# Kernel optimization log

Measured on AMD Instinct MI355X. Metric: run time of the kernel, lower is better.

## Reference

```python
import jax, jax.numpy as jnp
import numpy as np

D_MODEL = 2048
D_STATE = 128
D_CONV = 4
EXPAND = 2
HEADDIM = 64
NGROUPS = 1
CHUNK = 256
D_INNER = EXPAND * D_MODEL               # 4096 (= d_ssm, since d_ssm=None)
NHEADS = D_INNER // HEADDIM              # 64
CONV_DIM = D_INNER + 2 * NGROUPS * D_STATE   # 4352
D_IN_PROJ = 2 * D_INNER + 2 * NGROUPS * D_STATE + NHEADS  # 8512
EPS = 1e-5


def setup_inputs() -> dict:
    key = jax.random.key(0)
    ks = jax.random.split(key, 8)
    B, L = 2, 4096
    u = jax.random.normal(ks[0], (B, L, D_MODEL), jnp.float32)
    in_proj_kernel = jax.random.normal(ks[1], (D_MODEL, D_IN_PROJ), jnp.float32) * (1.0 / np.sqrt(D_MODEL))
    conv1d_weight = jax.random.normal(ks[2], (CONV_DIM, D_CONV), jnp.float32) * (1.0 / np.sqrt(D_CONV))
    conv1d_bias = jnp.zeros((CONV_DIM,), jnp.float32)
    # dt_bias: inverse-softplus of log-uniform dt in [dt_min, dt_max]
    uu = jax.random.uniform(ks[3], (NHEADS,), jnp.float32)
    dt = jnp.exp(uu * (np.log(0.1) - np.log(0.001)) + np.log(0.001))
    dt = jnp.maximum(dt, 1e-4)
    dt_bias = dt + jnp.log(-jnp.expm1(-dt))
    # A_log: log of uniform(1, 16)
    A_log = jnp.log(jax.random.uniform(ks[4], (NHEADS,), jnp.float32, minval=1.0, maxval=16.0))
    D = jnp.ones((NHEADS,), jnp.float32)
    norm_weight = jnp.ones((D_INNER,), jnp.float32)
    out_proj_kernel = jax.random.normal(ks[5], (D_INNER, D_MODEL), jnp.float32) * (1.0 / np.sqrt(D_INNER))
    return {"u": u, "in_proj_kernel": in_proj_kernel, "conv1d_weight": conv1d_weight,
            "conv1d_bias": conv1d_bias, "dt_bias": dt_bias, "A_log": A_log, "D": D,
            "norm_weight": norm_weight, "out_proj_kernel": out_proj_kernel}


def _segsum(x):
    """x: (..., L). Returns (..., L, L) with seg[i,j] = sum_{k=j+1..i} x_k for i>=j, -inf above diag."""
    T = x.shape[-1]
    cs = jnp.cumsum(x, axis=-1)
    seg = cs[..., :, None] - cs[..., None, :]
    mask = jnp.tril(jnp.ones((T, T), dtype=bool))
    return jnp.where(mask, seg, -jnp.inf)


def _causal_conv1d_silu(x, w, b):
    """Depthwise causal conv. x: (B, C, L), w: (C, K), b: (C,)."""
    K = w.shape[-1]
    Lx = x.shape[-1]
    xp = jnp.pad(x, ((0, 0), (0, 0), (K - 1, 0)))
    y = b[None, :, None]
    for k in range(K):  # K=4, tiny static loop
        y = y + w[None, :, k:k + 1] * xp[:, :, k:k + Lx]
    return jax.nn.silu(y)


def _mamba2_forward(u, in_proj_kernel, conv1d_weight, conv1d_bias, dt_bias, A_log, D,
                    norm_weight, out_proj_kernel):
    B_, L, _ = u.shape
    zxbcdt = u @ in_proj_kernel  # (B, L, d_in_proj); d_mlp = 0 so no z0/x0
    z = zxbcdt[..., :D_INNER]
    xBC = zxbcdt[..., D_INNER:D_INNER + CONV_DIM]
    dt = zxbcdt[..., D_INNER + CONV_DIM:]  # (B, L, H)

    xBC = _causal_conv1d_silu(jnp.transpose(xBC, (0, 2, 1)), conv1d_weight, conv1d_bias)
    xBC = jnp.transpose(xBC, (0, 2, 1))

    x = xBC[..., :D_INNER].reshape(B_, L, NHEADS, HEADDIM)
    Bm = xBC[..., D_INNER:D_INNER + NGROUPS * D_STATE].reshape(B_, L, NGROUPS, D_STATE)
    Cm = xBC[..., D_INNER + NGROUPS * D_STATE:].reshape(B_, L, NGROUPS, D_STATE)

    dt = jax.nn.softplus(dt + dt_bias)         # (B, L, H); dt_limit=(0,inf) => no clamp
    A = -jnp.exp(A_log)                        # (H,)

    nc = L // CHUNK
    r = NHEADS // NGROUPS
    # chunked views
    xc = x.reshape(B_, nc, CHUNK, NGROUPS, r, HEADDIM)
    dtc = dt.reshape(B_, nc, CHUNK, NGROUPS, r)
    Bc = Bm.reshape(B_, nc, CHUNK, NGROUPS, D_STATE)
    Cc = Cm.reshape(B_, nc, CHUNK, NGROUPS, D_STATE)
    xdt = xc * dtc[..., None]                  # dt-discretized input

    dA = dtc * A.reshape(NGROUPS, r)           # (B, nc, CL, g, r)
    dA = jnp.transpose(dA, (0, 3, 4, 1, 2))    # (B, g, r, nc, CL)
    A_cs = jnp.cumsum(dA, axis=-1)

    # intra-chunk (diagonal blocks)
    Lmat = jnp.exp(_segsum(dA))                # (B, g, r, nc, CL, CL)
    Y_diag = jnp.einsum('bclgn,bcsgn,bgrcls,bcsgrp->bclgrp', Cc, Bc, Lmat, xdt)

    # per-chunk end states
    decay_states = jnp.exp(A_cs[..., -1:] - A_cs)  # (B, g, r, nc, CL)
    states = jnp.einsum('bcsgn,bgrcs,bcsgrp->bcgrpn', Bc, decay_states, xdt)

    # inter-chunk recurrence over nc chunks
    chunk_decay = jnp.exp(A_cs[..., -1])       # (B, g, r, nc)
    states_t = jnp.moveaxis(states, 1, 0)      # (nc, B, g, r, p, n)
    decay_t = jnp.moveaxis(chunk_decay, -1, 0) # (nc, B, g, r)

    def step(S, inp):
        d, st = inp
        S_new = S * d[..., None, None] + st
        return S_new, S  # emit state at start of each chunk

    S0 = jnp.zeros(states_t.shape[1:], states_t.dtype)
    _, prev_states = jax.lax.scan(step, S0, (decay_t, states_t))
    prev_states = jnp.moveaxis(prev_states, 0, 1)  # (B, nc, g, r, p, n)

    state_decay = jnp.exp(A_cs)                # (B, g, r, nc, CL)
    Y_off = jnp.einsum('bclgn,bcgrpn,bgrcl->bclgrp', Cc, prev_states, state_decay)

    Y = (Y_diag + Y_off).reshape(B_, nc, CHUNK, NHEADS, HEADDIM)
    Y = Y + x.reshape(B_, nc, CHUNK, NHEADS, HEADDIM) * D[:, None]  # D skip (D_has_hdim=False)
    y = Y.reshape(B_, L, D_INNER)

    # RMSNormGated (norm_before_gate=False): norm(y * silu(z)) * weight
    y = y * jax.nn.silu(z)
    y = y * jax.lax.rsqrt(jnp.mean(y * y, axis=-1, keepdims=True) + EPS) * norm_weight

    return y @ out_proj_kernel


def reference(u, in_proj_kernel, conv1d_weight, conv1d_bias, dt_bias, A_log, D,
              norm_weight, out_proj_kernel):
    return _mamba2_forward(u, in_proj_kernel, conv1d_weight, conv1d_bias, dt_bias, A_log, D,
                           norm_weight, out_proj_kernel)
```

## Files before the change

### kernel.cpp

```cpp
#include <hip/hip_runtime.h>
#include <cstddef>
#include <cstdint>
#include <math.h>

#define BATCH   2
#define LSEQ    4096
#define DMODEL  2048
#define DSTATE  128
#define HDIM    64
#define CHUNK   256
#define DINNER  4096
#define NHEADS  64
#define CONVD   4352
#define DPROJ   8512
#define NCHUNK  16
#define MROWS   (BATCH*LSEQ)
#define NPAD2   8704

typedef unsigned short bf16_t;
union U4 { uint4 u; unsigned short s[8]; };

typedef __attribute__((ext_vector_type(8))) short short8;
typedef __attribute__((ext_vector_type(4))) float f32x4;
union S8 { short8 v; unsigned short s[8]; };

__device__ __forceinline__ float b2f(unsigned short u) {
    union { unsigned int i; float f; } v; v.i = ((unsigned int)u) << 16; return v.f;
}
__device__ __forceinline__ unsigned short f2b(float f) {
    union { float f; unsigned int i; } v; v.f = f;
    unsigned int r = v.i + 0x7fffu + ((v.i >> 16) & 1u);
    return (unsigned short)(r >> 16);
}

__device__ __forceinline__ void gload_lds16(const void* g, void* l) {
    auto gp = reinterpret_cast<const __attribute__((address_space(1))) unsigned int*>(
        reinterpret_cast<uintptr_t>(g));
    auto lp = reinterpret_cast<__attribute__((address_space(3))) unsigned int*>(
        reinterpret_cast<uintptr_t>(l));
    __builtin_amdgcn_global_load_lds(gp, lp, 16, 0, 0);
}

__global__ __launch_bounds__(256) void cast_bf16(const float* __restrict__ in,
                                                 bf16_t* __restrict__ out, size_t n8) {
    size_t i = (size_t)blockIdx.x * 256 + threadIdx.x;
    if (i >= n8) return;
    const float4 a = *(const float4*)(in + i * 8);
    const float4 b = *(const float4*)(in + i * 8 + 4);
    U4 o;
    o.s[0]=f2b(a.x); o.s[1]=f2b(a.y); o.s[2]=f2b(a.z); o.s[3]=f2b(a.w);
    o.s[4]=f2b(b.x); o.s[5]=f2b(b.y); o.s[6]=f2b(b.z); o.s[7]=f2b(b.w);
    *(uint4*)(out + i * 8) = o.u;
}

__global__ __launch_bounds__(256) void transpose_cast(const float* __restrict__ W,
                                                      bf16_t* __restrict__ Bt,
                                                      int K, int N) {
    __shared__ float t[32][33];
    const int bx = blockIdx.x;
    const int by = blockIdx.y;
    const int tx = threadIdx.x, ty = threadIdx.y;
    const int n = bx * 32 + tx;
#pragma unroll
    for (int r = 0; r < 4; ++r) {
        int k = by * 32 + ty + r * 8;
        t[ty + r * 8][tx] = (n < N) ? W[(size_t)k * N + n] : 0.f;
    }
    __syncthreads();
#pragma unroll
    for (int r = 0; r < 4; ++r) {
        int nn = bx * 32 + ty + r * 8;
        Bt[(size_t)nn * K + by * 32 + tx] = f2b(t[tx][ty + r * 8]);
    }
}

#define MM(a,b,c) __builtin_amdgcn_mfma_f32_16x16x32_bf16(a,b,c,0,0,0)

template<bool BF16OUT>
__global__ __launch_bounds__(512, 2) void gemm256(const bf16_t* __restrict__ A,
                                                  const bf16_t* __restrict__ Bt,
                                                  void* __restrict__ Cout,
                                                  int GX, int N, int K,
                                                  int lda, int ldb, int ldc) {
    __shared__ __align__(16) bf16_t Asm[2][256 * 64];
    __shared__ __align__(16) bf16_t Bsm[2][256 * 64];
    const int tid  = threadIdx.x;
    const int wid  = tid >> 6;
    const int lane = tid & 63;
    const int wm = wid >> 2;
    const int wn = wid & 3;

    const int nwg = gridDim.x;
    const int wg  = blockIdx.x;
    const int q8 = nwg >> 3, r8 = nwg & 7;
    const int xcd = wg & 7, lo = wg >> 3;
    const int swz = (xcd < r8 ? xcd * (q8 + 1) : r8 * (q8 + 1) + (xcd - r8) * q8) + lo;
    const int bm = (swz / GX) * 256;
    const int bn = (swz % GX) * 256;

    const int fr  = lane & 15;
    const int kx0 = ((((lane >> 4))     ^ (lane & 7)) * 8);
    const int kx1 = ((((lane >> 4) + 4) ^ (lane & 7)) * 8);
    const int laneA  = lane >> 3;
    const int chunkS = ((lane & 7) ^ (lane >> 3)) * 8;

    f32x4 acc[8][4];
#pragma unroll
    for (int i = 0; i < 8; ++i)
#pragma unroll
        for (int j = 0; j < 4; ++j) acc[i][j] = (f32x4){0.f, 0.f, 0.f, 0.f};

    short8 b00, b01, b10, b11, b20, b21, b30, b31;

#define STAGE_A(d, t, h) do { \
    const int r0_ = (h) * 128 + wid * 16; \
    gload_lds16(A + (size_t)(bm + r0_ +     laneA) * lda + (t) * 64 + chunkS, &Asm[d][(r0_    ) * 64]); \
    gload_lds16(A + (size_t)(bm + r0_ + 8 + laneA) * lda + (t) * 64 + chunkS, &Asm[d][(r0_ + 8) * 64]); \
} while (0)
#define STAGE_B(d, t, h) do { \
    const int r0_ = (h) * 128 + wid * 16; \
    gload_lds16(Bt + (size_t)(bn + r0_ +     laneA) * ldb + (t) * 64 + chunkS, &Bsm[d][(r0_    ) * 64]); \
    gload_lds16(Bt + (size_t)(bn + r0_ + 8 + laneA) * ldb + (t) * 64 + chunkS, &Bsm[d][(r0_ + 8) * 64]); \
} while (0)

#define PHASE(curb, qq, DOVM, ...) do { \
    const bf16_t* Ab_ = &Asm[curb][(wm * 128 + (qq) * 32 + fr) * 64]; \
    short8 a00 = *(const short8*)(Ab_ + kx0); \
    short8 a01 = *(const short8*)(Ab_ + kx1); \
    short8 a10 = *(const short8*)(Ab_ + 16 * 64 + kx0); \
    short8 a11 = *(const short8*)(Ab_ + 16 * 64 + kx1); \
    if ((qq) == 0) { \
        const bf16_t* Bb_ = &Bsm[curb][(wn * 64 + fr) * 64]; \
        b00 = *(const short8*)(Bb_ + kx0);           b01 = *(const short8*)(Bb_ + kx1); \
        b10 = *(const short8*)(Bb_ + 16 * 64 + kx0); b11 = *(const short8*)(Bb_ + 16 * 64 + kx1); \
        b20 = *(const short8*)(Bb_ + 32 * 64 + kx0); b21 = *(const short8*)(Bb_ + 32 * 64 + kx1); \
        b30 = *(const short8*)(Bb_ + 48 * 64 + kx0); b31 = *(const short8*)(Bb_ + 48 * 64 + kx1); \
    } \
    __VA_ARGS__ \
    __builtin_amdgcn_sched_barrier(0); \
    __builtin_amdgcn_s_barrier(); \
    asm volatile("s_waitcnt lgkmcnt(0)" ::: "memory"); \
    __builtin_amdgcn_sched_barrier(0); \
    __builtin_amdgcn_s_setprio(1); \
    acc[(qq)*2  ][0] = MM(a00, b00, acc[(qq)*2  ][0]); acc[(qq)*2  ][0] = MM(a01, b01, acc[(qq)*2  ][0]); \
    acc[(qq)*2  ][1] = MM(a00, b10, acc[(qq)*2  ][1]); acc[(qq)*2  ][1] = MM(a01, b11, acc[(qq)*2  ][1]); \
    acc[(qq)*2  ][2] = MM(a00, b20, acc[(qq)*2  ][2]); acc[(qq)*2  ][2] = MM(a01, b21, acc[(qq)*2  ][2]); \
    acc[(qq)*2  ][3] = MM(a00, b30, acc[(qq)*2  ][3]); acc[(qq)*2  ][3] = MM(a01, b31, acc[(qq)*2  ][3]); \
    acc[(qq)*2+1][0] = MM(a10, b00, acc[(qq)*2+1][0]); acc[(qq)*2+1][0] = MM(a11, b01, acc[(qq)*2+1][0]); \
    acc[(qq)*2+1][1] = MM(a10, b10, acc[(qq)*2+1][1]); acc[(qq)*2+1][1] = MM(a11, b11, acc[(qq)*2+1][1]); \
    acc[(qq)*2+1][2] = MM(a10, b20, acc[(qq)*2+1][2]); acc[(qq)*2+1][2] = MM(a11, b21, acc[(qq)*2+1][2]); \
    acc[(qq)*2+1][3] = MM(a10, b30, acc[(qq)*2+1][3]); acc[(qq)*2+1][3] = MM(a11, b31, acc[(qq)*2+1][3]); \
    __builtin_amdgcn_s_setprio(0); \
    __builtin_amdgcn_sched_barrier(0); \
    if ((DOVM) == 1)      asm volatile("s_waitcnt vmcnt(4)" ::: "memory"); \
    else if ((DOVM) == 2) asm volatile("s_waitcnt vmcnt(0)" ::: "memory"); \
    __builtin_amdgcn_s_barrier(); \
} while (0)

    const int NT = K >> 6;
    const int NI = NT >> 1;

    STAGE_A(0, 0, 0); STAGE_A(0, 0, 1);
    STAGE_B(0, 0, 0); STAGE_B(0, 0, 1);
    STAGE_B(1, 1, 0); STAGE_B(1, 1, 1);
    asm volatile("s_waitcnt vmcnt(4)" ::: "memory");
    __builtin_amdgcn_s_barrier();

    for (int i = 0; i < NI - 1; ++i) {
        const int t0 = 2 * i;
        PHASE(0, 0, 0, STAGE_A(1, t0 + 1, 0); );
        PHASE(0, 1, 0, STAGE_A(1, t0 + 1, 1); );
        PHASE(0, 2, 0, STAGE_B(0, t0 + 2, 0); );
        PHASE(0, 3, 1, STAGE_B(0, t0 + 2, 1); );
        PHASE(1, 0, 0, STAGE_A(0, t0 + 2, 0); );
        PHASE(1, 1, 0, STAGE_A(0, t0 + 2, 1); );
        PHASE(1, 2, 0, STAGE_B(1, t0 + 3, 0); );
        PHASE(1, 3, 1, STAGE_B(1, t0 + 3, 1); );
    }
    PHASE(0, 0, 0, STAGE_A(1, NT - 1, 0); );
    PHASE(0, 1, 0, STAGE_A(1, NT - 1, 1); );
    PHASE(0, 2, 0, );
    PHASE(0, 3, 2, );
    PHASE(1, 0, 0, );
    PHASE(1, 1, 0, );
    PHASE(1, 2, 0, );
    PHASE(1, 3, 0, );

#undef PHASE
#undef STAGE_A
#undef STAGE_B

    const int crow4 = (lane >> 4) * 4, ccol = lane & 15;
#pragma unroll
    for (int mr = 0; mr < 8; ++mr)
#pragma unroll
        for (int nf = 0; nf < 4; ++nf) {
            const int gr = bm + wm * 128 + mr * 16 + crow4;
            const int gc = bn + wn * 64 + nf * 16 + ccol;
            if (gc < N) {
                if (BF16OUT) {
                    bf16_t* C = (bf16_t*)Cout;
#pragma unroll
                    for (int r = 0; r < 4; ++r)
                        C[(size_t)(gr + r) * ldc + gc] = f2b(acc[mr][nf][r]);
                } else {
                    float* C = (float*)Cout;
#pragma unroll
                    for (int r = 0; r < 4; ++r)
                        C[(size_t)(gr + r) * ldc + gc] = acc[mr][nf][r];
                }
            }
        }
}

__global__ __launch_bounds__(256) void conv_silu(const bf16_t* __restrict__ zx,
                                                 const float* __restrict__ w,
                                                 const float* __restrict__ bias,
                                                 bf16_t* __restrict__ xconv) {
    const int c0 = (blockIdx.x * 256 + threadIdx.x) * 8;
    if (c0 >= CONVD) return;
    const int row0 = blockIdx.y * 4;
    float4 wv[8];
#pragma unroll
    for (int j = 0; j < 8; ++j) wv[j] = *(const float4*)(w + (size_t)(c0 + j) * 4);
    float bs[8];
    {
        float4 q0 = *(const float4*)(bias + c0), q1 = *(const float4*)(bias + c0 + 4);
        bs[0]=q0.x; bs[1]=q0.y; bs[2]=q0.z; bs[3]=q0.w;
        bs[4]=q1.x; bs[5]=q1.y; bs[6]=q1.z; bs[7]=q1.w;
    }
    U4 zin[7];
#pragma unroll
    for (int d = 0; d < 7; ++d) {
        int rr = row0 - 3 + d;
        if (rr >= 0) zin[d].u = *(const uint4*)(zx + (size_t)rr * DPROJ + DINNER + c0);
        else         zin[d].u = make_uint4(0, 0, 0, 0);
    }
    const int l0 = row0 & (LSEQ - 1);
#pragma unroll
    for (int r = 0; r < 4; ++r) {
        U4 o;
#pragma unroll
        for (int j = 0; j < 8; ++j) {
            float a = bs[j];
            const float* wj = (const float*)&wv[j];
#pragma unroll
            for (int k = 0; k < 4; ++k)
                if (l0 + r + k - 3 >= 0)
                    a += wj[k] * b2f(zin[r + k].s[j]);
            o.s[j] = f2b(a / (1.f + __expf(-a)));
        }
        *(uint4*)(xconv + (size_t)(row0 + r) * CONVD + c0) = o.u;
    }
}

__global__ void dt_softplus(const bf16_t* __restrict__ zx, const float* __restrict__ dt_bias,
                            float* __restrict__ dts) {
    const int idx = blockIdx.x * 256 + threadIdx.x;
    const int h = idx & 63;
    const int row = idx >> 6;
    float x = b2f(zx[(size_t)row * DPROJ + DINNER + CONVD + h]) + dt_bias[h];
    dts[idx] = (x > 20.f) ? x : log1pf(__expf(x));
}

__global__ __launch_bounds__(256) void chunk_state(const bf16_t* __restrict__ xconv,
                                                   const float* __restrict__ dts,
                                                   const float* __restrict__ A_log,
                                                   float* __restrict__ A_cs_g,
                                                   float* __restrict__ states) {
    const int h = blockIdx.x, cc = blockIdx.y, b = blockIdx.z;
    const int tid = threadIdx.x, wid = tid >> 6, lane = tid & 63;
    __shared__ float cs[CHUNK];
    __shared__ __align__(16) bf16_t xwT[HDIM][CHUNK + 8];
    __shared__ __align__(16) bf16_t BvT[DSTATE][CHUNK + 8];
    const int rowbase = b * LSEQ + cc * CHUNK;

    const float dtv = dts[(size_t)(rowbase + tid) * NHEADS + h];
    const float Ah = -__expf(A_log[h]);
    cs[tid] = dtv * Ah;
    __syncthreads();
    for (int off = 1; off < CHUNK; off <<= 1) {
        float v = (tid >= off) ? cs[tid - off] : 0.f;
        __syncthreads();
        cs[tid] += v;
        __syncthreads();
    }
    const size_t acs_base = ((size_t)((b * NCHUNK + cc) * NHEADS + h)) * CHUNK;
    A_cs_g[acs_base + tid] = cs[tid];
    const float w_ = __expf(cs[CHUNK - 1] - cs[tid]) * dtv;

    {
        const bf16_t* xr = xconv + (size_t)(rowbase + tid) * CONVD + h * HDIM;
#pragma unroll
        for (int p8 = 0; p8 < 8; ++p8) {
            U4 v; v.u = *(const uint4*)(xr + p8 * 8);
#pragma unroll
            for (int j = 0; j < 8; ++j) xwT[p8 * 8 + j][tid] = f2b(b2f(v.s[j]) * w_);
        }
        const bf16_t* br = xconv + (size_t)(rowbase + tid) * CONVD + DINNER;
#pragma unroll
        for (int n8 = 0; n8 < 16; ++n8) {
            U4 v; v.u = *(const uint4*)(br + n8 * 8);
#pragma unroll
            for (int j = 0; j < 8; ++j) BvT[n8 * 8 + j][tid] = v.s[j];
        }
    }
    __syncthreads();

    const int fr = lane & 15, fk8 = (lane >> 4) * 8;
    f32x4 acc[4][2];
#pragma unroll
    for (int i = 0; i < 4; ++i)
#pragma unroll
        for (int j = 0; j < 2; ++j) acc[i][j] = (f32x4){0.f, 0.f, 0.f, 0.f};

#pragma unroll
    for (int ks = 0; ks < 8; ++ks) {
        const int k0 = ks * 32 + fk8;
        short8 av[4], bv[2];
#pragma unroll
        for (int mi = 0; mi < 4; ++mi)
            av[mi] = *(const short8*)&xwT[mi * 16 + fr][k0];
#pragma unroll
        for (int ni = 0; ni < 2; ++ni)
            bv[ni] = *(const short8*)&BvT[wid * 32 + ni * 16 + fr][k0];
#pragma unroll
        for (int mi = 0; mi < 4; ++mi)
#pragma unroll
            for (int ni = 0; ni < 2; ++ni)
                acc[mi][ni] = __builtin_amdgcn_mfma_f32_16x16x32_bf16(
                    av[mi], bv[ni], acc[mi][ni], 0, 0, 0);
    }
    float* st = states + ((size_t)((b * NCHUNK + cc) * NHEADS + h)) * (HDIM * DSTATE);
    const int crow4 = (lane >> 4) * 4, ccol = lane & 15;
#pragma unroll
    for (int mi = 0; mi < 4; ++mi)
#pragma unroll
        for (int ni = 0; ni < 2; ++ni)
#pragma unroll
            for (int r = 0; r < 4; ++r)
                st[(size_t)(mi * 16 + crow4 + r) * DSTATE + wid * 32 + ni * 16 + ccol] =
                    acc[mi][ni][r];
}

__global__ __launch_bounds__(256) void state_scan(float* __restrict__ states,
                                                  const float* __restrict__ A_cs_g) {
    const int h = blockIdx.x, piece = blockIdx.y, b = blockIdx.z;
    const int tid = threadIdx.x;
    float S[4] = {0.f, 0.f, 0.f, 0.f};
    for (int c = 0; c < NCHUNK; ++c) {
        const size_t sbase = ((size_t)((b * NCHUNK + c) * NHEADS + h)) * (HDIM * DSTATE)
                           + (size_t)piece * 1024;
        const float decay = __expf(A_cs_g[((size_t)((b * NCHUNK + c) * NHEADS + h)) * CHUNK + CHUNK - 1]);
#pragma unroll
        for (int i = 0; i < 4; ++i) {
            size_t idx = sbase + i * 256 + tid;
            float v = states[idx];
            states[idx] = S[i];
            S[i] = S[i] * decay + v;
        }
    }
}

__global__ __launch_bounds__(256) void cb_mfma(const bf16_t* __restrict__ xconv,
                                               float* __restrict__ CBg) {
    const int pi = blockIdx.x, cc = blockIdx.y, b = blockIdx.z;
    const int lt = (pi >= 6) ? 3 : (pi >= 3) ? 2 : (pi >= 1) ? 1 : 0;
    const int st = pi - ((lt * (lt + 1)) >> 1);
    const int tid = threadIdx.x, wid = tid >> 6, lane = tid & 63;
    const int rowbase = b * LSEQ + cc * CHUNK;
    const int fr = lane & 15, fk8 = (lane >> 4) * 8;

    const bf16_t* Crow = xconv + (size_t)(rowbase + lt * 64 + wid * 16) * CONVD + DINNER + DSTATE;
    const bf16_t* Brow = xconv + (size_t)(rowbase + st * 64) * CONVD + DINNER;

    f32x4 acc[4];
#pragma unroll
    for (int i = 0; i < 4; ++i) acc[i] = (f32x4){0.f, 0.f, 0.f, 0.f};

#pragma unroll
    for (int kk = 0; kk < 4; ++kk) {
        const int k0 = kk * 32 + fk8;
        short8 av = *(const short8*)(Crow + (size_t)fr * CONVD + k0);
        short8 bv[4];
#pragma unroll
        for (int ni = 0; ni < 4; ++ni)
            bv[ni] = *(const short8*)(Brow + (size_t)(ni * 16 + fr) * CONVD + k0);
#pragma unroll
        for (int ni = 0; ni < 4; ++ni)
            acc[ni] = __builtin_amdgcn_mfma_f32_16x16x32_bf16(av, bv[ni], acc[ni], 0, 0, 0);
    }
    float* out = CBg + ((size_t)(b * NCHUNK + cc)) * CHUNK * CHUNK;
    const int crow4 = (lane >> 4) * 4, ccol = lane & 15;
#pragma unroll
    for (int ni = 0; ni < 4; ++ni)
#pragma unroll
        for (int r = 0; r < 4; ++r)
            out[(size_t)(lt * 64 + wid * 16 + crow4 + r) * CHUNK + st * 64 + ni * 16 + ccol] =
                acc[ni][r];
}

__global__ __launch_bounds__(256) void y_mfma(const bf16_t* __restrict__ xconv,
                                              const float* __restrict__ dts,
                                              const float* __restrict__ A_cs_g,
                                              const float* __restrict__ prev_states,
                                              const float* __restrict__ CBg,
                                              const float* __restrict__ Dv,
                                              bf16_t* __restrict__ zx) {
    const int h = blockIdx.x, cc = blockIdx.y, b = blockIdx.z;
    const int tid = threadIdx.x, wid = tid >> 6, lane = tid & 63;
    __shared__ float Acs_s[CHUNK];
    __shared__ __align__(16) bf16_t xdtT[HDIM][CHUNK + 8];
    __shared__ __align__(16) bf16_t Pt[4][64][72];
    const int rowbase = b * LSEQ + cc * CHUNK;
    const size_t acs_base = ((size_t)((b * NCHUNK + cc) * NHEADS + h)) * CHUNK;

    Acs_s[tid] = A_cs_g[acs_base + tid];
    {
        float dtv = dts[(size_t)(rowbase + tid) * NHEADS + h];
        const bf16_t* xr = xconv + (size_t)(rowbase + tid) * CONVD + h * HDIM;
#pragma unroll
        for (int p8 = 0; p8 < 8; ++p8) {
            U4 v; v.u = *(const uint4*)(xr + p8 * 8);
#pragma unroll
            for (int j = 0; j < 8; ++j)
                xdtT[p8 * 8 + j][tid] = f2b(b2f(v.s[j]) * dtv);
        }
    }
    __syncthreads();

    const int fr = lane & 15, fk8 = (lane >> 4) * 8;
    f32x4 acc[4][4];
#pragma unroll
    for (int i = 0; i < 4; ++i)
#pragma unroll
        for (int j = 0; j < 4; ++j) acc[i][j] = (f32x4){0.f, 0.f, 0.f, 0.f};

    const bf16_t* Crow = xconv + (size_t)(rowbase + wid * 64) * CONVD + DINNER + DSTATE;
    const float* prev = prev_states + ((size_t)((b * NCHUNK + cc) * NHEADS + h)) * (HDIM * DSTATE);
#pragma unroll
    for (int kk = 0; kk < 4; ++kk) {
        const int k0 = kk * 32 + fk8;
        short8 av[4], bv[4];
#pragma unroll
        for (int mi = 0; mi < 4; ++mi)
            av[mi] = *(const short8*)(Crow + (size_t)(mi * 16 + fr) * CONVD + k0);
#pragma unroll
        for (int ni = 0; ni < 4; ++ni) {
            const float* pr = prev + (size_t)(ni * 16 + fr) * DSTATE + k0;
            float4 f0 = *(const float4*)pr;
            float4 f1 = *(const float4*)(pr + 4);
            S8 t;
            t.s[0]=f2b(f0.x); t.s[1]=f2b(f0.y); t.s[2]=f2b(f0.z); t.s[3]=f2b(f0.w);
            t.s[4]=f2b(f1.x); t.s[5]=f2b(f1.y); t.s[6]=f2b(f1.z); t.s[7]=f2b(f1.w);
            bv[ni] = t.v;
        }
#pragma unroll
        for (int mi = 0; mi < 4; ++mi)
#pragma unroll
            for (int ni = 0; ni < 4; ++ni)
                acc[mi][ni] = __builtin_amdgcn_mfma_f32_16x16x32_bf16(
                    av[mi], bv[ni], acc[mi][ni], 0, 0, 0);
    }

    const int crow4 = (lane >> 4) * 4, ccol = lane & 15;
#pragma unroll
    for (int mi = 0; mi < 4; ++mi) {
        float e[4];
#pragma unroll
        for (int r = 0; r < 4; ++r)
            e[r] = __expf(Acs_s[wid * 64 + mi * 16 + crow4 + r]);
#pragma unroll
        for (int ni = 0; ni < 4; ++ni)
#pragma unroll
            for (int r = 0; r < 4; ++r) acc[mi][ni][r] *= e[r];
    }

    const float* cbb = CBg + ((size_t)(b * NCHUNK + cc)) * CHUNK * CHUNK;
    for (int st = 0; st <= wid; ++st) {
        const int s0 = st * 64;
        const float as_l = Acs_s[s0 + lane];
        __asm__ volatile("s_waitcnt lgkmcnt(0)" ::: "memory");
        __builtin_amdgcn_sched_barrier(0);
        for (int e = 0; e < 64; ++e) {
            const int gl = wid * 64 + e;
            float cbv = cbb[(size_t)gl * CHUNK + s0 + lane];
            float pv = cbv * __expf(Acs_s[gl] - as_l);
            if (st == wid && (s0 + lane) > gl) pv = 0.f;
            Pt[wid][e][lane] = f2b(pv);
        }
        __asm__ volatile("s_waitcnt lgkmcnt(0)" ::: "memory");
        __builtin_amdgcn_sched_barrier(0);
#pragma unroll
        for (int ks = 0; ks < 2; ++ks) {
            short8 av[4], bv[4];
#pragma unroll
            for (int mi = 0; mi < 4; ++mi)
                av[mi] = *(const short8*)&Pt[wid][mi * 16 + fr][ks * 32 + fk8];
#pragma unroll
            for (int ni = 0; ni < 4; ++ni)
                bv[ni] = *(const short8*)&xdtT[ni * 16 + fr][s0 + ks * 32 + fk8];
#pragma unroll
            for (int mi = 0; mi < 4; ++mi)
#pragma unroll
                for (int ni = 0; ni < 4; ++ni)
                    acc[mi][ni] = __builtin_amdgcn_mfma_f32_16x16x32_bf16(
                        av[mi], bv[ni], acc[mi][ni], 0, 0, 0);
        }
    }

    const float Dh = Dv[h];
#pragma unroll
    for (int mi = 0; mi < 4; ++mi)
#pragma unroll
        for (int ni = 0; ni < 4; ++ni) {
            const int p = ni * 16 + ccol;
#pragma unroll
            for (int r = 0; r < 4; ++r) {
                const int l = wid * 64 + mi * 16 + crow4 + r;
                const size_t row = (size_t)rowbase + l;
                float xr = b2f(xconv[row * CONVD + h * HDIM + p]);
                float zv = b2f(zx[row * DPROJ + h * HDIM + p]);
                float y = (acc[mi][ni][r] + xr * Dh) * (zv / (1.f + __expf(-zv)));
                zx[row * DPROJ + DINNER + h * HDIM + p] = f2b(y);
            }
        }
}

__global__ __launch_bounds__(256) void rmsnorm(bf16_t* __restrict__ zx, const float* __restrict__ nw) {
    const int row = blockIdx.x;
    const int tid = threadIdx.x;
    float fv[16];
    float ss = 0.f;
#pragma unroll
    for (int it = 0; it < 2; ++it) {
        int j0 = (it * 256 + tid) * 8;
        U4 v; v.u = *(const uint4*)(zx + (size_t)row * DPROJ + DINNER + j0);
#pragma unroll
        for (int j = 0; j < 8; ++j) { float f = b2f(v.s[j]); fv[it * 8 + j] = f; ss += f * f; }
    }
#pragma unroll
    for (int off = 32; off > 0; off >>= 1) ss += __shfl_down(ss, off, 64);
    __shared__ float red[4];
    if ((tid & 63) == 0) red[tid >> 6] = ss;
    __syncthreads();
    float tot = red[0] + red[1] + red[2] + red[3];
    float inv = rsqrtf(tot / (float)DINNER + 1e-5f);
#pragma unroll
    for (int it = 0; it < 2; ++it) {
        int j0 = (it * 256 + tid) * 8;
        U4 o;
#pragma unroll
        for (int j = 0; j < 8; ++j) o.s[j] = f2b(fv[it * 8 + j] * inv * nw[j0 + j]);
        *(uint4*)(zx + (size_t)row * DPROJ + j0) = o.u;
    }
}

extern "C" void kernel_launch(void* const* d_in, const int* in_sizes, int n_in,
                              void* d_out, int out_size, void* d_ws, size_t ws_size,
                              hipStream_t stream) {
    const float* u       = (const float*)d_in[0];
    const float* Win     = (const float*)d_in[1];
    const float* convw   = (const float*)d_in[2];
    const float* convb   = (const float*)d_in[3];
    const float* dt_bias = (const float*)d_in[4];
    const float* A_log   = (const float*)d_in[5];
    const float* Dv      = (const float*)d_in[6];
    const float* nw      = (const float*)d_in[7];
    const float* Wout    = (const float*)d_in[8];
    float* out = (float*)d_out;

    bf16_t* zx    = (bf16_t*)d_ws;
    bf16_t* xconv = zx + (size_t)MROWS * DPROJ;
    float*  dts   = (float*)(xconv + (size_t)MROWS * CONVD);
    float*  acs   = dts + (size_t)MROWS * NHEADS;
    float*  cb    = acs + (size_t)BATCH * NCHUNK * NHEADS * CHUNK;

    bf16_t* Abf    = xconv;
    bf16_t* Btin   = (bf16_t*)d_out;
    float*  states = (float*)d_out;
    bf16_t* Btout  = xconv;

    cast_bf16<<<(MROWS * DMODEL / 8 + 255) / 256, 256, 0, stream>>>(u, Abf, (size_t)MROWS * DMODEL / 8);
    transpose_cast<<<dim3(NPAD2 / 32, DMODEL / 32), dim3(32, 8), 0, stream>>>(Win, Btin, DMODEL, DPROJ);
    gemm256<true><<<dim3((NPAD2 / 256) * (MROWS / 256)), 512, 0, stream>>>(
        Abf, Btin, zx, NPAD2 / 256, DPROJ, DMODEL, DMODEL, DMODEL, DPROJ);
    conv_silu<<<dim3((CONVD / 8 + 255) / 256, MROWS / 4), 256, 0, stream>>>(zx, convw, convb, xconv);
    dt_softplus<<<dim3(MROWS * NHEADS / 256), 256, 0, stream>>>(zx, dt_bias, dts);
    chunk_state<<<dim3(NHEADS, NCHUNK, BATCH), 256, 0, stream>>>(xconv, dts, A_log, acs, states);
    state_scan<<<dim3(NHEADS, 8, BATCH), 256, 0, stream>>>(states, acs);
    cb_mfma<<<dim3(10, NCHUNK, BATCH), 256, 0, stream>>>(xconv, cb);
    y_mfma<<<dim3(NHEADS, NCHUNK, BATCH), 256, 0, stream>>>(xconv, dts, acs, states, cb, Dv, zx);
    transpose_cast<<<dim3(DMODEL / 32, DINNER / 32), dim3(32, 8), 0, stream>>>(Wout, Btout, DINNER, DMODEL);
    rmsnorm<<<MROWS, 256, 0, stream>>>(zx, nw);
    gemm256<false><<<dim3((DMODEL / 256) * (MROWS / 256)), 512, 0, stream>>>(
        zx, Btout, out, DMODEL / 256, DMODEL, DINNER, DPROJ, DINNER, DMODEL);
}
```

Before: 776.3 us.

## Triple-buffer A tiles in GEMM and reorder MFMAs to avoid accumulator stalls

The bf16 GEMM now keeps three LDS buffers for A instead of two, so A loads are issued two k-steps ahead and more global loads stay in flight (vmcnt relaxed from 4 to 8). The MFMA sequence is reordered so the two k-halves hitting the same accumulator are no longer back-to-back, hiding MFMA dependency latency. The explicit lgkmcnt(0) wait before the MFMAs is dropped, leaving LDS-read waits to the compiler. LDS use rises to 160 KB per block, which fills the CU's LDS and risks tighter scheduling or occupancy limits.

```diff
diff --git a/kernel.cpp b/kernel.cpp
--- a/kernel.cpp
+++ b/kernel.cpp
@@ -82,8 +82,9 @@
                                                   void* __restrict__ Cout,
                                                   int GX, int N, int K,
                                                   int lda, int ldb, int ldc) {
-    __shared__ __align__(16) bf16_t Asm[2][256 * 64];
-    __shared__ __align__(16) bf16_t Bsm[2][256 * 64];
+    __shared__ __align__(16) bf16_t Asm[3 * 256 * 64];
+    __shared__ __align__(16) bf16_t Bsm[2 * 256 * 64];
+    const int TSZ = 256 * 64;
     const int tid  = threadIdx.x;
     const int wid  = tid >> 6;
     const int lane = tid & 63;
@@ -112,25 +113,25 @@
 
     short8 b00, b01, b10, b11, b20, b21, b30, b31;
 
-#define STAGE_A(d, t, h) do { \
+#define STAGE_A(dst, t, h) do { \
     const int r0_ = (h) * 128 + wid * 16; \
-    gload_lds16(A + (size_t)(bm + r0_ +     laneA) * lda + (t) * 64 + chunkS, &Asm[d][(r0_    ) * 64]); \
-    gload_lds16(A + (size_t)(bm + r0_ + 8 + laneA) * lda + (t) * 64 + chunkS, &Asm[d][(r0_ + 8) * 64]); \
+    gload_lds16(A + (size_t)(bm + r0_ +     laneA) * lda + (t) * 64 + chunkS, (dst) + (r0_    ) * 64); \
+    gload_lds16(A + (size_t)(bm + r0_ + 8 + laneA) * lda + (t) * 64 + chunkS, (dst) + (r0_ + 8) * 64); \
 } while (0)
-#define STAGE_B(d, t, h) do { \
+#define STAGE_B(dst, t, h) do { \
     const int r0_ = (h) * 128 + wid * 16; \
-    gload_lds16(Bt + (size_t)(bn + r0_ +     laneA) * ldb + (t) * 64 + chunkS, &Bsm[d][(r0_    ) * 64]); \
-    gload_lds16(Bt + (size_t)(bn + r0_ + 8 + laneA) * ldb + (t) * 64 + chunkS, &Bsm[d][(r0_ + 8) * 64]); \
+    gload_lds16(Bt + (size_t)(bn + r0_ +     laneA) * ldb + (t) * 64 + chunkS, (dst) + (r0_    ) * 64); \
+    gload_lds16(Bt + (size_t)(bn + r0_ + 8 + laneA) * ldb + (t) * 64 + chunkS, (dst) + (r0_ + 8) * 64); \
 } while (0)
 
-#define PHASE(curb, qq, DOVM, ...) do { \
-    const bf16_t* Ab_ = &Asm[curb][(wm * 128 + (qq) * 32 + fr) * 64]; \
+#define PHASE(APTR, BPTR, qq, DOVM, ...) do { \
+    const bf16_t* Ab_ = (APTR) + (wm * 128 + (qq) * 32 + fr) * 64; \
     short8 a00 = *(const short8*)(Ab_ + kx0); \
     short8 a01 = *(const short8*)(Ab_ + kx1); \
     short8 a10 = *(const short8*)(Ab_ + 16 * 64 + kx0); \
     short8 a11 = *(const short8*)(Ab_ + 16 * 64 + kx1); \
     if ((qq) == 0) { \
-        const bf16_t* Bb_ = &Bsm[curb][(wn * 64 + fr) * 64]; \
+        const bf16_t* Bb_ = (BPTR) + (wn * 64 + fr) * 64; \
         b00 = *(const short8*)(Bb_ + kx0);           b01 = *(const short8*)(Bb_ + kx1); \
         b10 = *(const short8*)(Bb_ + 16 * 64 + kx0); b11 = *(const short8*)(Bb_ + 16 * 64 + kx1); \
         b20 = *(const short8*)(Bb_ + 32 * 64 + kx0); b21 = *(const short8*)(Bb_ + 32 * 64 + kx1); \
@@ -139,20 +140,26 @@
     __VA_ARGS__ \
     __builtin_amdgcn_sched_barrier(0); \
     __builtin_amdgcn_s_barrier(); \
-    asm volatile("s_waitcnt lgkmcnt(0)" ::: "memory"); \
-    __builtin_amdgcn_sched_barrier(0); \
     __builtin_amdgcn_s_setprio(1); \
-    acc[(qq)*2  ][0] = MM(a00, b00, acc[(qq)*2  ][0]); acc[(qq)*2  ][0] = MM(a01, b01, acc[(qq)*2  ][0]); \
-    acc[(qq)*2  ][1] = MM(a00, b10, acc[(qq)*2  ][1]); acc[(qq)*2  ][1] = MM(a01, b11, acc[(qq)*2  ][1]); \
-    acc[(qq)*2  ][2] = MM(a00, b20, acc[(qq)*2  ][2]); acc[(qq)*2  ][2] = MM(a01, b21, acc[(qq)*2  ][2]); \
-    acc[(qq)*2  ][3] = MM(a00, b30, acc[(qq)*2  ][3]); acc[(qq)*2  ][3] = MM(a01, b31, acc[(qq)*2  ][3]); \
-    acc[(qq)*2+1][0] = MM(a10, b00, acc[(qq)*2+1][0]); acc[(qq)*2+1][0] = MM(a11, b01, acc[(qq)*2+1][0]); \
-    acc[(qq)*2+1][1] = MM(a10, b10, acc[(qq)*2+1][1]); acc[(qq)*2+1][1] = MM(a11, b11, acc[(qq)*2+1][1]); \
-    acc[(qq)*2+1][2] = MM(a10, b20, acc[(qq)*2+1][2]); acc[(qq)*2+1][2] = MM(a11, b21, acc[(qq)*2+1][2]); \
-    acc[(qq)*2+1][3] = MM(a10, b30, acc[(qq)*2+1][3]); acc[(qq)*2+1][3] = MM(a11, b31, acc[(qq)*2+1][3]); \
+    acc[(qq)*2  ][0] = MM(a00, b00, acc[(qq)*2  ][0]); \
+    acc[(qq)*2  ][1] = MM(a00, b10, acc[(qq)*2  ][1]); \
+    acc[(qq)*2  ][2] = MM(a00, b20, acc[(qq)*2  ][2]); \
+    acc[(qq)*2  ][3] = MM(a00, b30, acc[(qq)*2  ][3]); \
+    acc[(qq)*2+1][0] = MM(a10, b00, acc[(qq)*2+1][0]); \
+    acc[(qq)*2+1][1] = MM(a10, b10, acc[(qq)*2+1][1]); \
+    acc[(qq)*2+1][2] = MM(a10, b20, acc[(qq)*2+1][2]); \
+    acc[(qq)*2+1][3] = MM(a10, b30, acc[(qq)*2+1][3]); \
+    acc[(qq)*2  ][0] = MM(a01, b01, acc[(qq)*2  ][0]); \
+    acc[(qq)*2  ][1] = MM(a01, b11, acc[(qq)*2  ][1]); \
+    acc[(qq)*2  ][2] = MM(a01, b21, acc[(qq)*2  ][2]); \
+    acc[(qq)*2  ][3] = MM(a01, b31, acc[(qq)*2  ][3]); \
+    acc[(qq)*2+1][0] = MM(a11, b01, acc[(qq)*2+1][0]); \
+    acc[(qq)*2+1][1] = MM(a11, b11, acc[(qq)*2+1][1]); \
+    acc[(qq)*2+1][2] = MM(a11, b21, acc[(qq)*2+1][2]); \
+    acc[(qq)*2+1][3] = MM(a11, b31, acc[(qq)*2+1][3]); \
     __builtin_amdgcn_s_setprio(0); \
     __builtin_amdgcn_sched_barrier(0); \
-    if ((DOVM) == 1)      asm volatile("s_waitcnt vmcnt(4)" ::: "memory"); \
+    if ((DOVM) == 1)      asm volatile("s_waitcnt vmcnt(8)" ::: "memory"); \
     else if ((DOVM) == 2) asm volatile("s_waitcnt vmcnt(0)" ::: "memory"); \
     __builtin_amdgcn_s_barrier(); \
 } while (0)
@@ -160,31 +167,41 @@
     const int NT = K >> 6;
     const int NI = NT >> 1;
 
-    STAGE_A(0, 0, 0); STAGE_A(0, 0, 1);
-    STAGE_B(0, 0, 0); STAGE_B(0, 0, 1);
-    STAGE_B(1, 1, 0); STAGE_B(1, 1, 1);
-    asm volatile("s_waitcnt vmcnt(4)" ::: "memory");
+    STAGE_A(Asm, 0, 0);       STAGE_A(Asm, 0, 1);
+    STAGE_B(Bsm, 0, 0);       STAGE_B(Bsm, 0, 1);
+    STAGE_A(Asm + TSZ, 1, 0); STAGE_A(Asm + TSZ, 1, 1);
+    STAGE_B(Bsm + TSZ, 1, 0); STAGE_B(Bsm + TSZ, 1, 1);
+    asm volatile("s_waitcnt vmcnt(8)" ::: "memory");
     __builtin_amdgcn_s_barrier();
 
+    int ac = 0;
     for (int i = 0; i < NI - 1; ++i) {
         const int t0 = 2 * i;
-        PHASE(0, 0, 0, STAGE_A(1, t0 + 1, 0); );
-        PHASE(0, 1, 0, STAGE_A(1, t0 + 1, 1); );
-        PHASE(0, 2, 0, STAGE_B(0, t0 + 2, 0); );
-        PHASE(0, 3, 1, STAGE_B(0, t0 + 2, 1); );
-        PHASE(1, 0, 0, STAGE_A(0, t0 + 2, 0); );
-        PHASE(1, 1, 0, STAGE_A(0, t0 + 2, 1); );
-        PHASE(1, 2, 0, STAGE_B(1, t0 + 3, 0); );
-        PHASE(1, 3, 1, STAGE_B(1, t0 + 3, 1); );
-    }
-    PHASE(0, 0, 0, STAGE_A(1, NT - 1, 0); );
-    PHASE(0, 1, 0, STAGE_A(1, NT - 1, 1); );
-    PHASE(0, 2, 0, );
-    PHASE(0, 3, 2, );
-    PHASE(1, 0, 0, );
-    PHASE(1, 1, 0, );
-    PHASE(1, 2, 0, );
-    PHASE(1, 3, 0, );
+        bf16_t* At  = Asm + ac * TSZ;
+        bf16_t* At1 = Asm + ((ac + 1) % 3) * TSZ;
+        bf16_t* At2 = Asm + ((ac + 2) % 3) * TSZ;
+        PHASE(At, Bsm, 0, 0, STAGE_A(At2, t0 + 2, 0); );
+        PHASE(At, Bsm, 1, 0, STAGE_A(At2, t0 + 2, 1); );
+        PHASE(At, Bsm, 2, 0, STAGE_B(Bsm, t0 + 2, 0); );
+        PHASE(At, Bsm, 3, 1, STAGE_B(Bsm, t0 + 2, 1); );
+        PHASE(At1, Bsm + TSZ, 0, 0, STAGE_A(At, t0 + 3, 0); );
+        PHASE(At1, Bsm + TSZ, 1, 0, STAGE_A(At, t0 + 3, 1); );
+        PHASE(At1, Bsm + TSZ, 2, 0, STAGE_B(Bsm + TSZ, t0 + 3, 0); );
+        PHASE(At1, Bsm + TSZ, 3, 1, STAGE_B(Bsm + TSZ, t0 + 3, 1); );
+        ac = (ac + 2) % 3;
+    }
+    {
+        bf16_t* At  = Asm + ac * TSZ;
+        bf16_t* At1 = Asm + ((ac + 1) % 3) * TSZ;
+        PHASE(At, Bsm, 0, 0, );
+        PHASE(At, Bsm, 1, 0, );
+        PHASE(At, Bsm, 2, 0, );
+        PHASE(At, Bsm, 3, 2, );
+        PHASE(At1, Bsm + TSZ, 0, 0, );
+        PHASE(At1, Bsm + TSZ, 1, 0, );
+        PHASE(At1, Bsm + TSZ, 2, 0, );
+        PHASE(At1, Bsm + TSZ, 3, 0, );
+    }
 
 #undef PHASE
 #undef STAGE_A
```

After: 782.4 us. About the same (+0.8%).

## Interleave chunk rows across waves in y_mfma to balance causal work

Applied to the files above, without the earlier changes.

Reassigns the 256 chunk rows in y_mfma so each wave takes a 16-row slice of every 64-row block instead of one contiguous 64-row block. The triangular intra-chunk work is then spread evenly across the four waves rather than leaving the last wave with four times the work of the first. The P staging buffer shrinks to 16 rows per wave. Separately, an explicit LDS wait after the barrier in the GEMM phase macro is removed, relying on compiler-inserted waits, which trims stalls but relaxes an explicit ordering guarantee.

```diff
diff --git a/kernel.cpp b/kernel.cpp
--- a/kernel.cpp
+++ b/kernel.cpp
@@ -139,8 +139,6 @@
     __VA_ARGS__ \
     __builtin_amdgcn_sched_barrier(0); \
     __builtin_amdgcn_s_barrier(); \
-    asm volatile("s_waitcnt lgkmcnt(0)" ::: "memory"); \
-    __builtin_amdgcn_sched_barrier(0); \
     __builtin_amdgcn_s_setprio(1); \
     acc[(qq)*2  ][0] = MM(a00, b00, acc[(qq)*2  ][0]); acc[(qq)*2  ][0] = MM(a01, b01, acc[(qq)*2  ][0]); \
     acc[(qq)*2  ][1] = MM(a00, b10, acc[(qq)*2  ][1]); acc[(qq)*2  ][1] = MM(a01, b11, acc[(qq)*2  ][1]); \
@@ -411,7 +409,7 @@
     const int tid = threadIdx.x, wid = tid >> 6, lane = tid & 63;
     __shared__ float Acs_s[CHUNK];
     __shared__ __align__(16) bf16_t xdtT[HDIM][CHUNK + 8];
-    __shared__ __align__(16) bf16_t Pt[4][64][72];
+    __shared__ __align__(16) bf16_t Pt[4][16][72];
     const int rowbase = b * LSEQ + cc * CHUNK;
     const size_t acs_base = ((size_t)((b * NCHUNK + cc) * NHEADS + h)) * CHUNK;
 
@@ -436,7 +434,7 @@
 #pragma unroll
         for (int j = 0; j < 4; ++j) acc[i][j] = (f32x4){0.f, 0.f, 0.f, 0.f};
 
-    const bf16_t* Crow = xconv + (size_t)(rowbase + wid * 64) * CONVD + DINNER + DSTATE;
+    const bf16_t* Cbase = xconv + (size_t)rowbase * CONVD + DINNER + DSTATE;
     const float* prev = prev_states + ((size_t)((b * NCHUNK + cc) * NHEADS + h)) * (HDIM * DSTATE);
 #pragma unroll
     for (int kk = 0; kk < 4; ++kk) {
@@ -444,7 +442,7 @@
         short8 av[4], bv[4];
 #pragma unroll
         for (int mi = 0; mi < 4; ++mi)
-            av[mi] = *(const short8*)(Crow + (size_t)(mi * 16 + fr) * CONVD + k0);
+            av[mi] = *(const short8*)(Cbase + (size_t)(mi * 64 + wid * 16 + fr) * CONVD + k0);
 #pragma unroll
         for (int ni = 0; ni < 4; ++ni) {
             const float* pr = prev + (size_t)(ni * 16 + fr) * DSTATE + k0;
@@ -469,7 +467,7 @@
         float e[4];
 #pragma unroll
         for (int r = 0; r < 4; ++r)
-            e[r] = __expf(Acs_s[wid * 64 + mi * 16 + crow4 + r]);
+            e[r] = __expf(Acs_s[mi * 64 + wid * 16 + crow4 + r]);
 #pragma unroll
         for (int ni = 0; ni < 4; ++ni)
 #pragma unroll
@@ -477,35 +475,37 @@
     }
 
     const float* cbb = CBg + ((size_t)(b * NCHUNK + cc)) * CHUNK * CHUNK;
-    for (int st = 0; st <= wid; ++st) {
-        const int s0 = st * 64;
-        const float as_l = Acs_s[s0 + lane];
-        __asm__ volatile("s_waitcnt lgkmcnt(0)" ::: "memory");
-        __builtin_amdgcn_sched_barrier(0);
-        for (int e = 0; e < 64; ++e) {
-            const int gl = wid * 64 + e;
-            float cbv = cbb[(size_t)gl * CHUNK + s0 + lane];
-            float pv = cbv * __expf(Acs_s[gl] - as_l);
-            if (st == wid && (s0 + lane) > gl) pv = 0.f;
-            Pt[wid][e][lane] = f2b(pv);
-        }
-        __asm__ volatile("s_waitcnt lgkmcnt(0)" ::: "memory");
-        __builtin_amdgcn_sched_barrier(0);
-#pragma unroll
-        for (int ks = 0; ks < 2; ++ks) {
-            short8 av[4], bv[4];
-#pragma unroll
-            for (int mi = 0; mi < 4; ++mi)
-                av[mi] = *(const short8*)&Pt[wid][mi * 16 + fr][ks * 32 + fk8];
-#pragma unroll
-            for (int ni = 0; ni < 4; ++ni)
-                bv[ni] = *(const short8*)&xdtT[ni * 16 + fr][s0 + ks * 32 + fk8];
-#pragma unroll
-            for (int mi = 0; mi < 4; ++mi)
+    bf16_t (*Pw)[72] = Pt[wid];
+#pragma unroll
+    for (int mi = 0; mi < 4; ++mi) {
+        const int lbase = mi * 64 + wid * 16;
+        for (int st = 0; st <= mi; ++st) {
+            const int s0 = st * 64;
+            const float as_l = Acs_s[s0 + lane];
+            __asm__ volatile("s_waitcnt lgkmcnt(0)" ::: "memory");
+            __builtin_amdgcn_sched_barrier(0);
+#pragma unroll
+            for (int e = 0; e < 16; ++e) {
+                const int gl = lbase + e;
+                float cbv = cbb[(size_t)gl * CHUNK + s0 + lane];
+                float pv = cbv * __expf(Acs_s[gl] - as_l);
+                if (st == mi && (s0 + lane) > gl) pv = 0.f;
+                Pw[e][lane] = f2b(pv);
+            }
+            __asm__ volatile("s_waitcnt lgkmcnt(0)" ::: "memory");
+            __builtin_amdgcn_sched_barrier(0);
+#pragma unroll
+            for (int ks = 0; ks < 2; ++ks) {
+                short8 av = *(const short8*)&Pw[fr][ks * 32 + fk8];
+                short8 bv[4];
+#pragma unroll
+                for (int ni = 0; ni < 4; ++ni)
+                    bv[ni] = *(const short8*)&xdtT[ni * 16 + fr][s0 + ks * 32 + fk8];
 #pragma unroll
                 for (int ni = 0; ni < 4; ++ni)
                     acc[mi][ni] = __builtin_amdgcn_mfma_f32_16x16x32_bf16(
-                        av[mi], bv[ni], acc[mi][ni], 0, 0, 0);
+                        av, bv[ni], acc[mi][ni], 0, 0, 0);
+            }
         }
     }
 
@@ -517,7 +517,7 @@
             const int p = ni * 16 + ccol;
 #pragma unroll
             for (int r = 0; r < 4; ++r) {
-                const int l = wid * 64 + mi * 16 + crow4 + r;
+                const int l = mi * 64 + wid * 16 + crow4 + r;
                 const size_t row = (size_t)rowbase + l;
                 float xr = b2f(xconv[row * CONVD + h * HDIM + p]);
                 float zv = b2f(zx[row * DPROJ + h * HDIM + p]);
```

Result: slower. 794.6 us (+2.4%).
